# Performance work log

Measured on AMD Instinct MI355X. Metric: run time of the kernel, lower is better.

Reference implementation:

```python
import jax, jax.numpy as jnp
import numpy as np

H = 1024          # hidden_size
E = 2 * H         # expansion e
S_DIM = 128       # shared q/k dim s
B, S = 4, 2048


def setup_inputs() -> dict:
    key = jax.random.key(0)
    ks = jax.random.split(key, 6)
    inputs = jax.random.normal(ks[0], (B, S, H), dtype=jnp.float32)
    W_uv = jax.random.normal(ks[1], (H, 2 * E + S_DIM), dtype=jnp.float32) * (1.0 / np.sqrt(H))
    b_uv = jnp.zeros((2 * E + S_DIM,), dtype=jnp.float32)
    gamma = jax.random.normal(ks[2], (2, S_DIM), dtype=jnp.float32) * 0.02
    beta = jnp.zeros((2, S_DIM), dtype=jnp.float32)
    W_out = jax.random.normal(ks[3], (E, H), dtype=jnp.float32) * (1.0 / np.sqrt(E))
    b_out = jnp.zeros((H,), dtype=jnp.float32)
    return {"inputs": inputs, "W_uv": W_uv, "b_uv": b_uv,
            "gamma": gamma, "beta": beta, "W_out": W_out, "b_out": b_out}


def reference(inputs, W_uv, b_uv, gamma, beta, W_out, b_out):
    seq_len = inputs.shape[1]
    # uv projection + SiLU
    uvb = jax.nn.silu(jnp.einsum('bsh,hf->bsf', inputs, W_uv) + b_uv)
    u = uvb[..., :E]                       # [B,S,E]
    v = uvb[..., E:2 * E]                  # [B,S,E]
    base = uvb[..., 2 * E:]                # [B,S,s]
    # per-head affine: [B,S,1,s]*[2,s] + [2,s] -> [B,S,2,s]
    qk = base[..., None, :] * gamma + beta
    q, k = qk[..., 0, :], qk[..., 1, :]    # [B,S,s] each
    scores = jnp.einsum('bns,bms->bnm', q, k) / seq_len   # [B,S,S]
    sq = jnp.square(jax.nn.relu(scores))
    attn_v = jnp.einsum('bnm,bme->bne', sq, v)            # [B,S,E]
    return jnp.einsum('bne,eh->bnh', u * attn_v, W_out) + b_out
```

## Files before the change

### kernel.cpp

```cpp
#include <hip/hip_runtime.h>
#include <stdint.h>


#define H_DIM  1024
#define E_DIM  2048
#define SD     128
#define B_SZ   4
#define S_LEN  2048
#define M_TOT  (B_SZ * S_LEN)
#define F_DIM  (2 * E_DIM + SD)

typedef _Float16 f16;
typedef __attribute__((ext_vector_type(4))) _Float16 f16x4;
typedef __attribute__((ext_vector_type(8))) _Float16 f16x8;
typedef __attribute__((ext_vector_type(16))) float f32x16;

__device__ __forceinline__ float silu_f(float x) { return x / (1.f + __expf(-x)); }

__device__ __forceinline__ void gload16(const void* g, void* l) {
  __builtin_amdgcn_global_load_lds(
      (const __attribute__((address_space(1))) void*)(uintptr_t)g,
      (__attribute__((address_space(3))) void*)(uint32_t)(uintptr_t)l,
      16, 0, 0);
}

__global__ __launch_bounds__(256) void cast_f16_k(const float* __restrict__ src,
                                                  f16* __restrict__ dst, long n) {
  long i = ((long)blockIdx.x * 256 + threadIdx.x) * 4;
  if (i < n) {
    float4 v = *(const float4*)(src + i);
    f16x4 h; h[0] = (f16)v.x; h[1] = (f16)v.y; h[2] = (f16)v.z; h[3] = (f16)v.w;
    *(f16x4*)(dst + i) = h;
  }
}

__global__ __launch_bounds__(256) void transpose_cast_k(const float* __restrict__ src,
                                                        f16* __restrict__ dst, int R, int C) {
  __shared__ float tile[32][33];
  int c0 = blockIdx.x * 32, r0 = blockIdx.y * 32;
  int tx = threadIdx.x & 31, ty = threadIdx.x >> 5;
  for (int i = ty; i < 32; i += 8) tile[i][tx] = src[(long)(r0 + i) * C + c0 + tx];
  __syncthreads();
  for (int i = ty; i < 32; i += 8) dst[(long)(c0 + i) * R + r0 + tx] = (f16)tile[tx][i];
}

template <int MODE>
__global__ __launch_bounds__(512, 2) void gemm256(
    const f16* __restrict__ Ag, const f16* __restrict__ Bg,
    float* __restrict__ F0, f16* __restrict__ O0, f16* __restrict__ O1,
    const f16* __restrict__ I0, const float* __restrict__ C0)
{
  constexpr int K  = (MODE == 0) ? H_DIM : 2048;
  constexpr int NT = K / 64;

  __shared__ f16 As[2][256][64];
  __shared__ f16 Bs[2][256][64];

  const int t    = threadIdx.x;
  const int w    = t >> 6;
  const int lane = t & 63;
  const int lo5  = lane & 31;
  const int hi   = lane >> 5;
  const int wm   = w >> 2;
  const int wn   = w & 3;

  const int gx  = gridDim.x;
  const int nwg = gx * gridDim.y;
  const int lin = blockIdx.y * gx + blockIdx.x;
  const int cpx = nwg >> 3;
  const int wg  = (lin & 7) * cpx + (lin >> 3);
  const int n0  = (wg % gx) * 256;
  const int m0  = (wg / gx) * 256;
  const long z  = blockIdx.z;

  const f16* A = Ag + (MODE == 2 ? z * (long)S_LEN * S_LEN : 0);
  const f16* B = Bg + (MODE == 2 ? z * (long)E_DIM * S_LEN : 0);

  auto stageA = [&](int bb, int half, int kt2) {
    const f16* g0 = A + (long)(m0 + half * 128) * K + kt2 * 64;
    f16* lb = &As[bb][half * 128][0];
#pragma unroll
    for (int j = 0; j < 2; j++) {
      int grp = (j << 3) + w;
      int rl  = (grp << 3) + (lane >> 3);
      gload16(g0 + (long)rl * K + (((lane & 7) ^ (lane >> 3)) << 3), lb + (grp << 9));
    }
  };
  auto stageB = [&](int bb, int half, int kt2) {
    const f16* g0 = B + (long)(n0 + half * 128) * K + kt2 * 64;
    f16* lb = &Bs[bb][half * 128][0];
#pragma unroll
    for (int j = 0; j < 2; j++) {
      int grp = (j << 3) + w;
      int rl  = (grp << 3) + (lane >> 3);
      gload16(g0 + (long)rl * K + (((lane & 7) ^ (lane >> 3)) << 3), lb + (grp << 9));
    }
  };

  f32x16 acc[4][2] = {};

  stageA(0, 0, 0); stageA(0, 1, 0); stageB(0, 0, 0); stageB(0, 1, 0);
  stageB(1, 0, 1); stageA(1, 1, 1);
  asm volatile("s_waitcnt vmcnt(4)" ::: "memory");
  __builtin_amdgcn_s_barrier();

#define PHASE(Q, MS, NS, STAGE_STMT, TAIL_STMT) do {                            \
    f16x8 av0_[4], av1_[4], bv_[4];                                             \
    const int ar_ = (MS) * 128 + wm * 64 + lo5;                                 \
    const int br_ = (NS) * 128 + wn * 32 + lo5;                                 \
    _Pragma("unroll")                                                           \
    for (int ksl = 0; ksl < 4; ksl++) {                                         \
      const int pc_ = (((ksl << 1) + hi) ^ (lo5 & 7)) << 3;                     \
      av0_[ksl] = *(const f16x8*)&As[bf][ar_][pc_];                             \
      av1_[ksl] = *(const f16x8*)&As[bf][ar_ + 32][pc_];                        \
      bv_[ksl]  = *(const f16x8*)&Bs[bf][br_][pc_];                             \
    }                                                                           \
    STAGE_STMT;                                                                 \
    __builtin_amdgcn_s_barrier();                                               \
    __builtin_amdgcn_s_setprio(1);                                              \
    _Pragma("unroll")                                                           \
    for (int ksl = 0; ksl < 4; ksl++) {                                         \
      acc[Q][0] = __builtin_amdgcn_mfma_f32_32x32x16_f16(av0_[ksl], bv_[ksl],   \
                                                         acc[Q][0], 0, 0, 0);   \
      acc[Q][1] = __builtin_amdgcn_mfma_f32_32x32x16_f16(av1_[ksl], bv_[ksl],   \
                                                         acc[Q][1], 0, 0, 0);   \
    }                                                                           \
    __builtin_amdgcn_s_setprio(0);                                              \
    TAIL_STMT;                                                                  \
    __builtin_amdgcn_s_barrier();                                               \
  } while (0)

  for (int kt = 0; kt < NT; ++kt) {
    const int bf = kt & 1;
    const bool s1 = (kt + 1 < NT);
    const bool s2 = (kt + 2 < NT);
    PHASE(0, 0, 0, if (s1) { stageA(bf ^ 1, 0, kt + 1); stageB(bf ^ 1, 1, kt + 1); }, );
    PHASE(1, 1, 0, , );
    PHASE(2, 1, 1, if (s2) { stageB(bf, 0, kt + 2); }, );
    PHASE(3, 0, 1, if (s2) { stageA(bf, 1, kt + 2); },
          if (s2) { asm volatile("s_waitcnt vmcnt(4)" ::: "memory"); }
          else    { asm volatile("s_waitcnt vmcnt(0)" ::: "memory"); });
  }
#undef PHASE

#pragma unroll
  for (int q = 0; q < 4; q++) {
    const int ms = (q == 1 || q == 2) ? 1 : 0;
    const int ns = q >> 1;
#pragma unroll
    for (int im = 0; im < 2; im++) {
      const int gc    = n0 + ns * 128 + wn * 32 + lo5;
      const int rbase = m0 + ms * 128 + wm * 64 + im * 32 + (hi << 2);
      if (MODE == 0) {
        const float bias = C0[gc];
        if (n0 < E_DIM) {
#pragma unroll
          for (int g = 0; g < 4; g++)
#pragma unroll
            for (int rr = 0; rr < 4; rr++) {
              int gr = rbase + (g << 3) + rr;
              O0[(long)gr * E_DIM + gc] = (f16)silu_f(acc[q][im][g * 4 + rr] + bias);
            }
        } else {
#pragma unroll
          for (int g = 0; g < 4; g++) {
            int gr0 = rbase + (g << 3);
            int b   = gr0 >> 11;
            int s0  = gr0 & (S_LEN - 1);
            f16x4 pk;
#pragma unroll
            for (int rr = 0; rr < 4; rr++) pk[rr] = (f16)silu_f(acc[q][im][g * 4 + rr] + bias);
            *(f16x4*)&O1[((long)b * E_DIM + (gc - E_DIM)) * S_LEN + s0] = pk;
          }
        }
      } else if (MODE == 2) {
        const long rowoff = z * S_LEN;
#pragma unroll
        for (int g = 0; g < 4; g++)
#pragma unroll
          for (int rr = 0; rr < 4; rr++) {
            int gr = rbase + (g << 3) + rr;
            long idx = (rowoff + gr) * (long)E_DIM + gc;
            O0[idx] = (f16)((float)I0[idx] * acc[q][im][g * 4 + rr]);
          }
      } else {
        const float bias = C0[gc];
#pragma unroll
        for (int g = 0; g < 4; g++)
#pragma unroll
          for (int rr = 0; rr < 4; rr++) {
            int gr = rbase + (g << 3) + rr;
            F0[(long)gr * H_DIM + gc] = acc[q][im][g * 4 + rr] * (1.0f / 17179869184.0f) + bias;
          }
      }
    }
  }
}

template <int MODE>
__global__ __launch_bounds__(256) void mfma_gemm(
    const f16* __restrict__ Ag, const f16* __restrict__ Bg,
    float* __restrict__ F0, f16* __restrict__ H0, const f16* __restrict__ H1,
    f16* __restrict__ H2, f16* __restrict__ H3,
    const float* __restrict__ C0, const float* __restrict__ C1,
    const float* __restrict__ C2)
{
  constexpr int K   = (MODE == 1) ? SD : H_DIM;
  constexpr int LDA = K, LDB = K;

  __shared__ f16 As[2][128][32];
  __shared__ f16 Bs[2][128][32];

  const int t    = threadIdx.x;
  const int w    = t >> 6;
  const int lane = t & 63;
  const int lo5  = lane & 31;
  const int hi   = lane >> 5;
  const int wy   = w >> 1, wx = w & 1;
  const int m0   = blockIdx.y * 128;
  const int n0   = blockIdx.x * 128;
  const long z   = blockIdx.z;

  const f16* A = Ag + (MODE == 1 ? z * (long)S_LEN * SD : 0);
  const f16* B = Bg + (MODE == 1 ? z * (long)S_LEN * SD : 0);

  const int srow = lane >> 2;
  const int scol = (((lane & 3) ^ ((srow >> 1) & 3))) * 8;
  const int rsw  = (lo5 >> 1) & 3;

  f32x16 acc[2][2] = {};

  for (int k0 = 0; k0 < K; k0 += 64) {
#pragma unroll
    for (int h = 0; h < 2; h++)
#pragma unroll
      for (int g16 = 0; g16 < 2; g16++) {
        const int r = (w << 5) + (g16 << 4);
        gload16(A + (long)(m0 + r + srow) * LDA + k0 + (h << 5) + scol, &As[h][r][0]);
        gload16(B + (long)(n0 + r + srow) * LDB + k0 + (h << 5) + scol, &Bs[h][r][0]);
      }
    __syncthreads();

#pragma unroll
    for (int ks = 0; ks < 4; ks++) {
      const int h  = ks >> 1;
      const int cl = ((ks & 1) << 1) + hi;
      const int kc = (cl ^ rsw) << 3;
      f16x8 av[2], bv[2];
#pragma unroll
      for (int i = 0; i < 2; i++)
        av[i] = *(const f16x8*)&As[h][(wy << 6) + (i << 5) + lo5][kc];
#pragma unroll
      for (int j = 0; j < 2; j++)
        bv[j] = *(const f16x8*)&Bs[h][(wx << 6) + (j << 5) + lo5][kc];
#pragma unroll
      for (int i = 0; i < 2; i++)
#pragma unroll
        for (int j = 0; j < 2; j++)
          acc[i][j] = __builtin_amdgcn_mfma_f32_32x32x16_f16(av[i], bv[j], acc[i][j], 0, 0, 0);
    }
    __syncthreads();
  }

  const int rb0 = m0 + (wy << 6) + (hi << 2);
  const int cb0 = n0 + (wx << 6) + lo5;

  if (MODE == 4) {
#pragma unroll
    for (int i = 0; i < 2; i++)
#pragma unroll
      for (int j = 0; j < 2; j++) {
        int jj = cb0 + (j << 5);
        float bias = C0[jj];
        float g0 = C1[jj], g1 = C1[SD + jj];
        float be0 = C2[jj], be1 = C2[SD + jj];
#pragma unroll
        for (int g = 0; g < 4; g++)
#pragma unroll
          for (int rr = 0; rr < 4; rr++) {
            int gr = rb0 + (i << 5) + (g << 3) + rr;
            float s = silu_f(acc[i][j][g * 4 + rr] + bias);
            H2[(long)gr * SD + jj] = (f16)(s * g0 + be0);
            H3[(long)gr * SD + jj] = (f16)(s * g1 + be1);
          }
      }
  } else {
#pragma unroll
    for (int i = 0; i < 2; i++)
#pragma unroll
      for (int j = 0; j < 2; j++) {
        int gc = cb0 + (j << 5);
#pragma unroll
        for (int g = 0; g < 4; g++)
#pragma unroll
          for (int rr = 0; rr < 4; rr++) {
            int gr = rb0 + (i << 5) + (g << 3) + rr;
            float tv = fmaxf(acc[i][j][g * 4 + rr], 0.f) * 64.f;
            H0[z * (long)S_LEN * S_LEN + (long)gr * S_LEN + gc] = (f16)(tv * tv);
          }
      }
  }
}

extern "C" void kernel_launch(void* const* d_in, const int* in_sizes, int n_in,
                              void* d_out, int out_size, void* d_ws, size_t ws_size,
                              hipStream_t stream) {
  const float* X     = (const float*)d_in[0];
  const float* W_uv  = (const float*)d_in[1];
  const float* b_uv  = (const float*)d_in[2];
  const float* gamma = (const float*)d_in[3];
  const float* beta  = (const float*)d_in[4];
  const float* W_out = (const float*)d_in[5];
  const float* b_out = (const float*)d_in[6];
  float* out = (float*)d_out;

  char* wp = (char*)d_ws;
  f16* Xh   = (f16*)wp; wp += (long)M_TOT * H_DIM * 2;
  f16* Wuvt = (f16*)wp; wp += (long)F_DIM * H_DIM * 2;
  f16* Wt   = (f16*)wp; wp += (long)H_DIM * E_DIM * 2;
  f16* u    = (f16*)wp; wp += (long)M_TOT * E_DIM * 2;
  f16* vt   = (f16*)wp; wp += (long)M_TOT * E_DIM * 2;
  f16* qh   = (f16*)wp; wp += (long)M_TOT * SD * 2;
  f16* kh   = (f16*)wp; wp += (long)M_TOT * SD * 2;
  f16* sq   = (f16*)wp; wp += (long)B_SZ * S_LEN * S_LEN * 2;
  f16* p    = (f16*)wp; wp += (long)M_TOT * E_DIM * 2;

  cast_f16_k<<<(M_TOT * H_DIM) / (256 * 4), 256, 0, stream>>>(X, Xh, (long)M_TOT * H_DIM);
  transpose_cast_k<<<dim3(F_DIM / 32, H_DIM / 32), 256, 0, stream>>>(W_uv, Wuvt, H_DIM, F_DIM);
  transpose_cast_k<<<dim3(H_DIM / 32, E_DIM / 32), 256, 0, stream>>>(W_out, Wt, E_DIM, H_DIM);

  gemm256<0><<<dim3(2 * E_DIM / 256, M_TOT / 256, 1), 512, 0, stream>>>(
      Xh, Wuvt, nullptr, u, vt, nullptr, b_uv);

  mfma_gemm<4><<<dim3(1, M_TOT / 128, 1), 256, 0, stream>>>(
      Xh, Wuvt + (long)2 * E_DIM * H_DIM, nullptr, nullptr, nullptr, qh, kh,
      b_uv + 2 * E_DIM, gamma, beta);

  mfma_gemm<1><<<dim3(S_LEN / 128, S_LEN / 128, B_SZ), 256, 0, stream>>>(
      qh, kh, nullptr, sq, nullptr, nullptr, nullptr, nullptr, nullptr, nullptr);

  gemm256<2><<<dim3(E_DIM / 256, S_LEN / 256, B_SZ), 512, 0, stream>>>(
      sq, vt, nullptr, p, nullptr, u, nullptr);

  gemm256<3><<<dim3(H_DIM / 256, M_TOT / 256, 1), 512, 0, stream>>>(
      p, Wt, out, nullptr, nullptr, nullptr, b_out);
}
```

Baseline: 435.2 us.

## Reuse LDS fragments across quadrants and deepen prefetch to two full tiles

Restructures the GEMM main loop so A and B fragments loaded from LDS are kept in registers and reused across the four output quadrants, instead of reloading both operands in every phase. The prologue now stages two full k-tiles, and the refill of each buffer half is rescheduled to go out as soon as its data has been read. A row-parity term is added to the XOR swizzle on both the global-to-LDS stores and the LDS reads, to cut LDS bank conflicts. In exchange the loop holds more fragment registers live, which may lower occupancy, and the quadrant-to-accumulator mapping in the epilogue is changed to match.

New measurement: 371.3 us. -14.7%, faster.

```diff
diff --git a/kernel.cpp b/kernel.cpp
--- a/kernel.cpp
+++ b/kernel.cpp
@@ -83,7 +83,8 @@
     for (int j = 0; j < 2; j++) {
       int grp = (j << 3) + w;
       int rl  = (grp << 3) + (lane >> 3);
-      gload16(g0 + (long)rl * K + (((lane & 7) ^ (lane >> 3)) << 3), lb + (grp << 9));
+      gload16(g0 + (long)rl * K + (((lane & 7) ^ (lane >> 3) ^ (grp & 1)) << 3),
+              lb + (grp << 9));
     }
   };
   auto stageB = [&](int bb, int half, int kt2) {
@@ -93,60 +94,95 @@
     for (int j = 0; j < 2; j++) {
       int grp = (j << 3) + w;
       int rl  = (grp << 3) + (lane >> 3);
-      gload16(g0 + (long)rl * K + (((lane & 7) ^ (lane >> 3)) << 3), lb + (grp << 9));
+      gload16(g0 + (long)rl * K + (((lane & 7) ^ (lane >> 3) ^ (grp & 1)) << 3),
+              lb + (grp << 9));
     }
   };
 
   f32x16 acc[4][2] = {};
+  f16x8 a0[2][4], a1[2][4], b0[4], b1[4];
+
+  const int swz = (lo5 & 7) ^ ((lo5 >> 3) & 1);
+  const int rA  = wm * 64 + lo5;
+  const int rB  = wn * 32 + lo5;
 
   stageA(0, 0, 0); stageA(0, 1, 0); stageB(0, 0, 0); stageB(0, 1, 0);
-  stageB(1, 0, 1); stageA(1, 1, 1);
-  asm volatile("s_waitcnt vmcnt(4)" ::: "memory");
+  stageA(1, 0, 1); stageA(1, 1, 1); stageB(1, 0, 1); stageB(1, 1, 1);
+  asm volatile("s_waitcnt vmcnt(8)" ::: "memory");
   __builtin_amdgcn_s_barrier();
-
-#define PHASE(Q, MS, NS, STAGE_STMT, TAIL_STMT) do {                            \
-    f16x8 av0_[4], av1_[4], bv_[4];                                             \
-    const int ar_ = (MS) * 128 + wm * 64 + lo5;                                 \
-    const int br_ = (NS) * 128 + wn * 32 + lo5;                                 \
-    _Pragma("unroll")                                                           \
-    for (int ksl = 0; ksl < 4; ksl++) {                                         \
-      const int pc_ = (((ksl << 1) + hi) ^ (lo5 & 7)) << 3;                     \
-      av0_[ksl] = *(const f16x8*)&As[bf][ar_][pc_];                             \
-      av1_[ksl] = *(const f16x8*)&As[bf][ar_ + 32][pc_];                        \
-      bv_[ksl]  = *(const f16x8*)&Bs[bf][br_][pc_];                             \
-    }                                                                           \
-    STAGE_STMT;                                                                 \
-    __builtin_amdgcn_s_barrier();                                               \
-    __builtin_amdgcn_s_setprio(1);                                              \
-    _Pragma("unroll")                                                           \
-    for (int ksl = 0; ksl < 4; ksl++) {                                         \
-      acc[Q][0] = __builtin_amdgcn_mfma_f32_32x32x16_f16(av0_[ksl], bv_[ksl],   \
-                                                         acc[Q][0], 0, 0, 0);   \
-      acc[Q][1] = __builtin_amdgcn_mfma_f32_32x32x16_f16(av1_[ksl], bv_[ksl],   \
-                                                         acc[Q][1], 0, 0, 0);   \
-    }                                                                           \
-    __builtin_amdgcn_s_setprio(0);                                              \
-    TAIL_STMT;                                                                  \
-    __builtin_amdgcn_s_barrier();                                               \
-  } while (0)
 
   for (int kt = 0; kt < NT; ++kt) {
     const int bf = kt & 1;
-    const bool s1 = (kt + 1 < NT);
     const bool s2 = (kt + 2 < NT);
-    PHASE(0, 0, 0, if (s1) { stageA(bf ^ 1, 0, kt + 1); stageB(bf ^ 1, 1, kt + 1); }, );
-    PHASE(1, 1, 0, , );
-    PHASE(2, 1, 1, if (s2) { stageB(bf, 0, kt + 2); }, );
-    PHASE(3, 0, 1, if (s2) { stageA(bf, 1, kt + 2); },
-          if (s2) { asm volatile("s_waitcnt vmcnt(4)" ::: "memory"); }
-          else    { asm volatile("s_waitcnt vmcnt(0)" ::: "memory"); });
-  }
-#undef PHASE
+
+#pragma unroll
+    for (int ksl = 0; ksl < 4; ksl++) {
+      const int pc = ((((ksl << 1) + hi) ^ swz) << 3);
+      a0[0][ksl] = *(const f16x8*)&As[bf][rA][pc];
+      a0[1][ksl] = *(const f16x8*)&As[bf][rA + 32][pc];
+      b0[ksl]    = *(const f16x8*)&Bs[bf][rB][pc];
+    }
+    __builtin_amdgcn_s_barrier();
+    __builtin_amdgcn_s_setprio(1);
+#pragma unroll
+    for (int ksl = 0; ksl < 4; ksl++) {
+      acc[0][0] = __builtin_amdgcn_mfma_f32_32x32x16_f16(a0[0][ksl], b0[ksl], acc[0][0], 0, 0, 0);
+      acc[0][1] = __builtin_amdgcn_mfma_f32_32x32x16_f16(a0[1][ksl], b0[ksl], acc[0][1], 0, 0, 0);
+    }
+    __builtin_amdgcn_s_setprio(0);
+    __builtin_amdgcn_s_barrier();
+
+    if (s2) { stageA(bf, 0, kt + 2); stageB(bf, 0, kt + 2); }
+#pragma unroll
+    for (int ksl = 0; ksl < 4; ksl++) {
+      const int pc = ((((ksl << 1) + hi) ^ swz) << 3);
+      b1[ksl] = *(const f16x8*)&Bs[bf][128 + rB][pc];
+    }
+    __builtin_amdgcn_s_barrier();
+    __builtin_amdgcn_s_setprio(1);
+#pragma unroll
+    for (int ksl = 0; ksl < 4; ksl++) {
+      acc[1][0] = __builtin_amdgcn_mfma_f32_32x32x16_f16(a0[0][ksl], b1[ksl], acc[1][0], 0, 0, 0);
+      acc[1][1] = __builtin_amdgcn_mfma_f32_32x32x16_f16(a0[1][ksl], b1[ksl], acc[1][1], 0, 0, 0);
+    }
+    __builtin_amdgcn_s_setprio(0);
+    __builtin_amdgcn_s_barrier();
+
+    if (s2) stageB(bf, 1, kt + 2);
+#pragma unroll
+    for (int ksl = 0; ksl < 4; ksl++) {
+      const int pc = ((((ksl << 1) + hi) ^ swz) << 3);
+      a1[0][ksl] = *(const f16x8*)&As[bf][128 + rA][pc];
+      a1[1][ksl] = *(const f16x8*)&As[bf][128 + rA + 32][pc];
+    }
+    __builtin_amdgcn_s_barrier();
+    __builtin_amdgcn_s_setprio(1);
+#pragma unroll
+    for (int ksl = 0; ksl < 4; ksl++) {
+      acc[3][0] = __builtin_amdgcn_mfma_f32_32x32x16_f16(a1[0][ksl], b1[ksl], acc[3][0], 0, 0, 0);
+      acc[3][1] = __builtin_amdgcn_mfma_f32_32x32x16_f16(a1[1][ksl], b1[ksl], acc[3][1], 0, 0, 0);
+    }
+    __builtin_amdgcn_s_setprio(0);
+    __builtin_amdgcn_s_barrier();
+
+    if (s2) stageA(bf, 1, kt + 2);
+    __builtin_amdgcn_s_barrier();
+    __builtin_amdgcn_s_setprio(1);
+#pragma unroll
+    for (int ksl = 0; ksl < 4; ksl++) {
+      acc[2][0] = __builtin_amdgcn_mfma_f32_32x32x16_f16(a1[0][ksl], b0[ksl], acc[2][0], 0, 0, 0);
+      acc[2][1] = __builtin_amdgcn_mfma_f32_32x32x16_f16(a1[1][ksl], b0[ksl], acc[2][1], 0, 0, 0);
+    }
+    __builtin_amdgcn_s_setprio(0);
+    if (s2) { asm volatile("s_waitcnt vmcnt(8)" ::: "memory"); }
+    else    { asm volatile("s_waitcnt vmcnt(0)" ::: "memory"); }
+    __builtin_amdgcn_s_barrier();
+  }
 
 #pragma unroll
   for (int q = 0; q < 4; q++) {
-    const int ms = (q == 1 || q == 2) ? 1 : 0;
-    const int ns = q >> 1;
+    const int ms = q >> 1;
+    const int ns = q & 1;
 #pragma unroll
     for (int im = 0; im < 2; im++) {
       const int gc    = n0 + ns * 128 + wn * 32 + lo5;
```
